# Performance work log

Measured on AMD Instinct MI355X. Metric: run time of the kernel, lower is better.

The kernel has to match this reference:

```python
import jax, jax.numpy as jnp
import numpy as np

N_NODES = 100000
N_EDGES = 1600000
N_GRAPHS = 1024
HID = 128
FINAL = 128
SPATIAL = 3
NUM_LAYERS = 3
VOCAB = 100


def _linear_params(key, d_in, d_out):
    k1, k2 = jax.random.split(key)
    s = 1.0 / np.sqrt(d_in)
    W = jax.random.uniform(k1, (d_out, d_in), jnp.float32, -s, s)
    b = jax.random.uniform(k2, (d_out,), jnp.float32, -s, s)
    return W, b


def setup_inputs() -> dict:
    key = jax.random.key(0)
    ks = jax.random.split(key, 16)
    z = jax.random.randint(ks[0], (N_NODES,), 0, VOCAB)
    pos = jax.random.normal(ks[1], (N_NODES, SPATIAL), jnp.float32)
    edge_index = jax.random.randint(ks[2], (2, N_EDGES), 0, N_NODES)
    batch = jnp.sort(jax.random.randint(ks[3], (N_NODES,), 0, N_GRAPHS))
    emb_table = jax.random.normal(ks[4], (VOCAB, HID), jnp.float32)
    W_pos, b_pos = _linear_params(ks[5], SPATIAL, HID)
    W_comb, b_comb = _linear_params(ks[6], 2 * HID, HID)
    # GIN: each conv's MLP is Linear(d,d) -> ReLU -> Linear(d,d); all dims 128 here.
    gW1, gb1, gW2, gb2 = [], [], [], []
    for i in range(NUM_LAYERS):
        k = jax.random.fold_in(ks[7], i)
        ka, kb = jax.random.split(k)
        W1, b1 = _linear_params(ka, HID, HID)
        W2, b2 = _linear_params(kb, HID, FINAL if i == NUM_LAYERS - 1 else HID)
        gW1.append(W1); gb1.append(b1); gW2.append(W2); gb2.append(b2)
    gin_W1 = jnp.stack(gW1); gin_b1 = jnp.stack(gb1)
    gin_W2 = jnp.stack(gW2); gin_b2 = jnp.stack(gb2)
    W_p1, b_p1 = _linear_params(ks[8], FINAL, FINAL)
    W_p2, b_p2 = _linear_params(ks[9], FINAL, 1)
    return {
        "z": z, "pos": pos, "edge_index": edge_index, "batch": batch,
        "emb_table": emb_table, "W_pos": W_pos, "b_pos": b_pos,
        "W_comb": W_comb, "b_comb": b_comb,
        "gin_W1": gin_W1, "gin_b1": gin_b1, "gin_W2": gin_W2, "gin_b2": gin_b2,
        "W_p1": W_p1, "b_p1": b_p1, "W_p2": W_p2, "b_p2": b_p2,
    }


def reference(z, pos, edge_index, batch, emb_table, W_pos, b_pos, W_comb, b_comb,
              gin_W1, gin_b1, gin_W2, gin_b2, W_p1, b_p1, W_p2, b_p2):
    src, dst = edge_index[0], edge_index[1]
    # initial node embedding: embed(z) || linear(pos) -> linear -> relu
    atom = emb_table[z]                                   # [N, H]
    pe = pos @ W_pos.T + b_pos                            # [N, H]
    x = jax.nn.relu(jnp.concatenate([atom, pe], axis=-1) @ W_comb.T + b_comb)
    # GIN layers: x' = MLP((1+eps)*x + sum_{j->i} x_j), eps=0; act between convs only
    for i in range(NUM_LAYERS):
        aggr = jax.ops.segment_sum(x[src], dst, num_segments=N_NODES)  # [N, H]
        h = aggr + x
        h = jax.nn.relu(h @ gin_W1[i].T + gin_b1[i])
        x = h @ gin_W2[i].T + gin_b2[i]
        if i < NUM_LAYERS - 1:
            x = jax.nn.relu(x)
    # sum pooling per graph, then predict MLP
    g = jax.ops.segment_sum(x, batch, num_segments=N_GRAPHS)  # [G, F]
    h = jax.nn.relu(g @ W_p1.T + b_p1)
    return h @ W_p2.T + b_p2                              # [G, 1]
```

## Files before the change

kernel.cpp:

```cpp
#include <hip/hip_runtime.h>
#include <hip/hip_bf16.h>

#define HID 128
#define CAP 64
#define NBK 2048
#define NWC 192

typedef __attribute__((ext_vector_type(8))) short bfrag;
typedef __attribute__((ext_vector_type(4))) float f32x4;

static inline size_t align256(size_t x) { return (x + 255) & ~(size_t)255; }

__device__ __forceinline__ unsigned short f2bf(float f) {
  unsigned int x = __float_as_uint(f);
  unsigned int r = x + 0x7fffu + ((x >> 16) & 1u);
  return (unsigned short)(r >> 16);
}
__device__ __forceinline__ float bflo(unsigned int u) { return __uint_as_float(u << 16); }
__device__ __forceinline__ float bfhi(unsigned int u) { return __uint_as_float(u & 0xffff0000u); }

__device__ __forceinline__ bfrag load8bf(const float* __restrict__ p) {
  const float4 a = *(const float4*)p;
  const float4 b = *(const float4*)(p + 4);
  bfrag r;
  r[0] = (short)f2bf(a.x); r[1] = (short)f2bf(a.y);
  r[2] = (short)f2bf(a.z); r[3] = (short)f2bf(a.w);
  r[4] = (short)f2bf(b.x); r[5] = (short)f2bf(b.y);
  r[6] = (short)f2bf(b.z); r[7] = (short)f2bf(b.w);
  return r;
}


__global__ __launch_bounds__(256, 2) void k_mega(
    const int* __restrict__ src, const int* __restrict__ dst,
    int* __restrict__ cnt, int* __restrict__ bsrc, int E, int N,
    const float* __restrict__ gW1, const float* __restrict__ gW2,
    unsigned short* __restrict__ W1b, unsigned short* __restrict__ W2b,
    const int* __restrict__ batch, int* __restrict__ goff, int G, int initBase,
    const int* __restrict__ z, const float* __restrict__ pos,
    const float* __restrict__ emb, const float* __restrict__ W_pos,
    const float* __restrict__ b_pos, const float* __restrict__ W_comb,
    const float* __restrict__ b_comb,
    unsigned int* __restrict__ UbZ, unsigned int* __restrict__ VbZ,
    unsigned short* __restrict__ Y, int n) {
  __shared__ unsigned int sE[32 * 128];
  __shared__ unsigned int sB[32 * 64];
  const int bid = blockIdx.x;
  const int tid = threadIdx.x;

  if (bid < NBK) {
    const int slice = bid & 7;
    const int sidx = bid >> 3;
    const int s_lo = (int)(((long long)slice * N) >> 3);
    const int s_hi = (int)(((long long)(slice + 1) * N) >> 3);
    for (int e = sidx * 256 + tid; e < E; e += (NBK / 8) * 256) {
      int d = dst[e];
      if (d >= s_lo && d < s_hi) {
        int slot = atomicAdd(&cnt[d], 1);
        if (slot < CAP) bsrc[(size_t)d * CAP + slot] = src[e];
      }
    }
    return;
  }
  if (bid < NBK + NWC) {
    int i = (bid - NBK) * 256 + tid;
    if (i < 3 * 128 * 128) {
      W1b[i] = f2bf(gW1[i]);
      W2b[i] = f2bf(gW2[i]);
    }
    return;
  }
  if (bid < initBase) {
    int g = (bid - NBK - NWC) * 256 + tid;
    if (g <= G) {
      int lo = 0, hi = N;
      while (lo < hi) {
        int mid = (lo + hi) >> 1;
        if (batch[mid] < g) lo = mid + 1; else hi = mid;
      }
      goff[g] = lo;
    }
    if (bid == initBase - 1) {
      if (tid >= 64 && tid < 128) UbZ[tid - 64] = 0;
      else if (tid >= 128 && tid < 192) VbZ[tid - 128] = 0;
    }
    return;
  }

  const int w = tid >> 6, l = tid & 63, lr = l & 15, lk = l >> 4;

  bfrag wcf[2][8];
#pragma unroll
  for (int s = 0; s < 2; ++s)
#pragma unroll
    for (int ks = 0; ks < 8; ++ks)
      wcf[s][ks] = load8bf(&W_comb[(size_t)(32 * w + 16 * s + lr) * 256 + ks * 32 + lk * 8]);
  bfrag w1f[2][4];
#pragma unroll
  for (int s = 0; s < 2; ++s)
#pragma unroll
    for (int ks = 0; ks < 4; ++ks)
      w1f[s][ks] = load8bf(&gW1[(size_t)(32 * w + 16 * s + lr) * HID + ks * 32 + lk * 8]);
  const float bias0 = b_comb[32 * w + lr];
  const float bias1 = b_comb[32 * w + 16 + lr];

  const int m0 = (bid - initBase) * 32;
  {
    const int r = tid >> 3, i = tid & 7;
    int node = m0 + r;
    if (node >= n) node = n - 1;
    const int zz = z[node];
    const float p0 = pos[node * 3 + 0], p1 = pos[node * 3 + 1], p2 = pos[node * 3 + 2];
    const int swz = (r & 7) << 2;
#pragma unroll
    for (int k = 0; k < 16; ++k) {
      const int j = i + k * 8;
      float v0, v1;
      if (j < 64) {
        const float2 ev = *(const float2*)&emb[(size_t)zz * 128 + 2 * j];
        v0 = ev.x; v1 = ev.y;
      } else {
        const int f0 = 2 * j - 128;
        v0 = b_pos[f0] + W_pos[f0 * 3] * p0 + W_pos[f0 * 3 + 1] * p1 + W_pos[f0 * 3 + 2] * p2;
        v1 = b_pos[f0 + 1] + W_pos[f0 * 3 + 3] * p0 + W_pos[f0 * 3 + 4] * p1 +
             W_pos[f0 * 3 + 5] * p2;
      }
      sE[r * 128 + (j ^ swz)] = (unsigned int)f2bf(v0) | ((unsigned int)f2bf(v1) << 16);
    }
  }
  __syncthreads();

  f32x4 acc00 = {0.f, 0.f, 0.f, 0.f}, acc01 = acc00, acc10 = acc00, acc11 = acc00;
#pragma unroll
  for (int mt = 0; mt < 2; ++mt) {
    const int row = 16 * mt + lr;
    const int swz = (row & 7) << 2;
#pragma unroll
    for (int ks = 0; ks < 8; ++ks) {
      const bfrag a = *(const bfrag*)&sE[row * 128 + ((ks * 16 + lk * 4) ^ swz)];
      if (mt == 0) {
        acc00 = __builtin_amdgcn_mfma_f32_16x16x32_bf16(a, wcf[0][ks], acc00, 0, 0, 0);
        acc01 = __builtin_amdgcn_mfma_f32_16x16x32_bf16(a, wcf[1][ks], acc01, 0, 0, 0);
      } else {
        acc10 = __builtin_amdgcn_mfma_f32_16x16x32_bf16(a, wcf[0][ks], acc10, 0, 0, 0);
        acc11 = __builtin_amdgcn_mfma_f32_16x16x32_bf16(a, wcf[1][ks], acc11, 0, 0, 0);
      }
    }
  }
  {
    unsigned short* sB16 = (unsigned short*)sB;
#pragma unroll
    for (int mt = 0; mt < 2; ++mt) {
#pragma unroll
      for (int s = 0; s < 2; ++s) {
        const f32x4 a = mt == 0 ? (s == 0 ? acc00 : acc01) : (s == 0 ? acc10 : acc11);
        const float bb = s == 0 ? bias0 : bias1;
        const int col = 32 * w + 16 * s + lr;
#pragma unroll
        for (int r = 0; r < 4; ++r) {
          const int rowL = 16 * mt + 4 * lk + r;
          const int cu = (col >> 1) ^ ((rowL & 7) << 2);
          sB16[rowL * 128 + cu * 2 + (col & 1)] = f2bf(fmaxf(a[r] + bb, 0.f));
        }
      }
    }
  }
  __syncthreads();

  f32x4 u00 = {0.f, 0.f, 0.f, 0.f}, u01 = u00, u10 = u00, u11 = u00;
#pragma unroll
  for (int mt = 0; mt < 2; ++mt) {
    const int row = 16 * mt + lr;
    const int swz = (row & 7) << 2;
#pragma unroll
    for (int ks = 0; ks < 4; ++ks) {
      const bfrag a = *(const bfrag*)&sB[row * 64 + ((ks * 16 + lk * 4) ^ swz)];
      if (mt == 0) {
        u00 = __builtin_amdgcn_mfma_f32_16x16x32_bf16(a, w1f[0][ks], u00, 0, 0, 0);
        u01 = __builtin_amdgcn_mfma_f32_16x16x32_bf16(a, w1f[1][ks], u01, 0, 0, 0);
      } else {
        u10 = __builtin_amdgcn_mfma_f32_16x16x32_bf16(a, w1f[0][ks], u10, 0, 0, 0);
        u11 = __builtin_amdgcn_mfma_f32_16x16x32_bf16(a, w1f[1][ks], u11, 0, 0, 0);
      }
    }
  }
#pragma unroll
  for (int mt = 0; mt < 2; ++mt) {
#pragma unroll
    for (int s = 0; s < 2; ++s) {
      const f32x4 a = mt == 0 ? (s == 0 ? u00 : u01) : (s == 0 ? u10 : u11);
      const int col = 32 * w + 16 * s + lr;
#pragma unroll
      for (int r = 0; r < 4; ++r) {
        const int row = m0 + 16 * mt + 4 * lk + r;
        if (row < n) Y[(size_t)row * HID + col] = f2bf(a[r]);
      }
    }
  }
}


template <int LAST>
__global__ __launch_bounds__(256, 3) void k_layer(const unsigned int* __restrict__ U,
                                                  const int* __restrict__ cnt,
                                                  const int* __restrict__ bsrc,
                                                  const float* __restrict__ b1,
                                                  const unsigned short* __restrict__ W2b,
                                                  const float* __restrict__ b2,
                                                  const unsigned short* __restrict__ W1n,
                                                  unsigned short* __restrict__ Y, int n) {
  __shared__ unsigned int sA[32 * 64];
  __shared__ unsigned int sB[32 * 64];
  const int t = threadIdx.x;
  const int w = t >> 6, l = t & 63, lr = l & 15, lk = l >> 4;
  const int lgrp = lk, lpos = lr;

  bfrag w2f[2][4];
#pragma unroll
  for (int s = 0; s < 2; ++s)
#pragma unroll
    for (int ks = 0; ks < 4; ++ks)
      w2f[s][ks] = *(const bfrag*)(W2b + (size_t)(32 * w + 16 * s + lr) * HID + ks * 32 + lk * 8);
  bfrag w1f[2][4];
  if (!LAST) {
#pragma unroll
    for (int s = 0; s < 2; ++s)
#pragma unroll
      for (int ks = 0; ks < 4; ++ks)
        w1f[s][ks] = *(const bfrag*)(W1n + (size_t)(32 * w + 16 * s + lr) * HID + ks * 32 + lk * 8);
  }
  const float b2a = b2[32 * w + lr];
  const float b2b = b2[32 * w + 16 + lr];
  const float4 bb0 = *(const float4*)&b1[8 * lpos];
  const float4 bb1 = *(const float4*)&b1[8 * lpos + 4];
  const float ms = (lgrp == 0) ? 1.f : 0.f;

  const int m0 = blockIdx.x * 32;

  int degs[8];
  int eidxs[8];
#pragma unroll
  for (int ri = 0; ri < 8; ++ri) {
    int node = m0 + 8 * w + ri;
    if (node >= n) node = n - 1;
    int d = cnt[node];
    d = d > CAP ? CAP : d;
    degs[ri] = d;
    const int e = bsrc[(size_t)node * CAP + l];
    eidxs[ri] = (l < d) ? e : n;
  }
#pragma unroll
  for (int ri = 0; ri < 8; ++ri) {
    const int row = 8 * w + ri;
    int node = m0 + row;
    if (node >= n) node = n - 1;
    const int deg8 = (degs[ri] + 7) & ~7;
    const int eidx = eidxs[ri];
    const uint4 sv = *(const uint4*)(U + (size_t)node * 64 + 4 * lpos);
    float a0 = ms * bflo(sv.x), a1 = ms * bfhi(sv.x);
    float a2 = ms * bflo(sv.y), a3 = ms * bfhi(sv.y);
    float a4 = ms * bflo(sv.z), a5 = ms * bfhi(sv.z);
    float a6 = ms * bflo(sv.w), a7 = ms * bfhi(sv.w);
    for (int k = 0; k < deg8; k += 8) {
      const int e0 = __shfl(eidx, k + lgrp);
      const int e1 = __shfl(eidx, k + 4 + lgrp);
      const uint4 u0 = *(const uint4*)(U + (size_t)e0 * 64 + 4 * lpos);
      const uint4 u1 = *(const uint4*)(U + (size_t)e1 * 64 + 4 * lpos);
      a0 += bflo(u0.x); a1 += bfhi(u0.x); a2 += bflo(u0.y); a3 += bfhi(u0.y);
      a4 += bflo(u0.z); a5 += bfhi(u0.z); a6 += bflo(u0.w); a7 += bfhi(u0.w);
      a0 += bflo(u1.x); a1 += bfhi(u1.x); a2 += bflo(u1.y); a3 += bfhi(u1.y);
      a4 += bflo(u1.z); a5 += bfhi(u1.z); a6 += bflo(u1.w); a7 += bfhi(u1.w);
    }
    a0 += __shfl_xor(a0, 16); a0 += __shfl_xor(a0, 32);
    a1 += __shfl_xor(a1, 16); a1 += __shfl_xor(a1, 32);
    a2 += __shfl_xor(a2, 16); a2 += __shfl_xor(a2, 32);
    a3 += __shfl_xor(a3, 16); a3 += __shfl_xor(a3, 32);
    a4 += __shfl_xor(a4, 16); a4 += __shfl_xor(a4, 32);
    a5 += __shfl_xor(a5, 16); a5 += __shfl_xor(a5, 32);
    a6 += __shfl_xor(a6, 16); a6 += __shfl_xor(a6, 32);
    a7 += __shfl_xor(a7, 16); a7 += __shfl_xor(a7, 32);
    if (lgrp == 0) {
      const int swz = (row & 7) << 2;
      uint4 o;
      o.x = (unsigned int)f2bf(fmaxf(a0 + bb0.x, 0.f)) |
            ((unsigned int)f2bf(fmaxf(a1 + bb0.y, 0.f)) << 16);
      o.y = (unsigned int)f2bf(fmaxf(a2 + bb0.z, 0.f)) |
            ((unsigned int)f2bf(fmaxf(a3 + bb0.w, 0.f)) << 16);
      o.z = (unsigned int)f2bf(fmaxf(a4 + bb1.x, 0.f)) |
            ((unsigned int)f2bf(fmaxf(a5 + bb1.y, 0.f)) << 16);
      o.w = (unsigned int)f2bf(fmaxf(a6 + bb1.z, 0.f)) |
            ((unsigned int)f2bf(fmaxf(a7 + bb1.w, 0.f)) << 16);
      *(uint4*)&sA[row * 64 + ((4 * lpos) ^ swz)] = o;
    }
  }
  __syncthreads();

  f32x4 acc00 = {0.f, 0.f, 0.f, 0.f}, acc01 = acc00, acc10 = acc00, acc11 = acc00;
#pragma unroll
  for (int mt = 0; mt < 2; ++mt) {
    const int row = 16 * mt + lr;
    const int swz = (row & 7) << 2;
#pragma unroll
    for (int ks = 0; ks < 4; ++ks) {
      const bfrag a = *(const bfrag*)&sA[row * 64 + ((ks * 16 + lk * 4) ^ swz)];
      if (mt == 0) {
        acc00 = __builtin_amdgcn_mfma_f32_16x16x32_bf16(a, w2f[0][ks], acc00, 0, 0, 0);
        acc01 = __builtin_amdgcn_mfma_f32_16x16x32_bf16(a, w2f[1][ks], acc01, 0, 0, 0);
      } else {
        acc10 = __builtin_amdgcn_mfma_f32_16x16x32_bf16(a, w2f[0][ks], acc10, 0, 0, 0);
        acc11 = __builtin_amdgcn_mfma_f32_16x16x32_bf16(a, w2f[1][ks], acc11, 0, 0, 0);
      }
    }
  }
  if (LAST) {
#pragma unroll
    for (int mt = 0; mt < 2; ++mt) {
#pragma unroll
      for (int s = 0; s < 2; ++s) {
        const f32x4 a = mt == 0 ? (s == 0 ? acc00 : acc01) : (s == 0 ? acc10 : acc11);
        const float bb = s == 0 ? b2a : b2b;
        const int col = 32 * w + 16 * s + lr;
#pragma unroll
        for (int r = 0; r < 4; ++r) {
          const int row = m0 + 16 * mt + 4 * lk + r;
          if (row < n) Y[(size_t)row * HID + col] = f2bf(a[r] + bb);
        }
      }
    }
  } else {
    unsigned short* sB16 = (unsigned short*)sB;
#pragma unroll
    for (int mt = 0; mt < 2; ++mt) {
#pragma unroll
      for (int s = 0; s < 2; ++s) {
        const f32x4 a = mt == 0 ? (s == 0 ? acc00 : acc01) : (s == 0 ? acc10 : acc11);
        const float bb = s == 0 ? b2a : b2b;
        const int col = 32 * w + 16 * s + lr;
#pragma unroll
        for (int r = 0; r < 4; ++r) {
          const int rowL = 16 * mt + 4 * lk + r;
          const int cu = (col >> 1) ^ ((rowL & 7) << 2);
          sB16[rowL * 128 + cu * 2 + (col & 1)] = f2bf(fmaxf(a[r] + bb, 0.f));
        }
      }
    }
    __syncthreads();
    f32x4 u00 = {0.f, 0.f, 0.f, 0.f}, u01 = u00, u10 = u00, u11 = u00;
#pragma unroll
    for (int mt = 0; mt < 2; ++mt) {
      const int row = 16 * mt + lr;
      const int swz = (row & 7) << 2;
#pragma unroll
      for (int ks = 0; ks < 4; ++ks) {
        const bfrag a = *(const bfrag*)&sB[row * 64 + ((ks * 16 + lk * 4) ^ swz)];
        if (mt == 0) {
          u00 = __builtin_amdgcn_mfma_f32_16x16x32_bf16(a, w1f[0][ks], u00, 0, 0, 0);
          u01 = __builtin_amdgcn_mfma_f32_16x16x32_bf16(a, w1f[1][ks], u01, 0, 0, 0);
        } else {
          u10 = __builtin_amdgcn_mfma_f32_16x16x32_bf16(a, w1f[0][ks], u10, 0, 0, 0);
          u11 = __builtin_amdgcn_mfma_f32_16x16x32_bf16(a, w1f[1][ks], u11, 0, 0, 0);
        }
      }
    }
#pragma unroll
    for (int mt = 0; mt < 2; ++mt) {
#pragma unroll
      for (int s = 0; s < 2; ++s) {
        const f32x4 a = mt == 0 ? (s == 0 ? u00 : u01) : (s == 0 ? u10 : u11);
        const int col = 32 * w + 16 * s + lr;
#pragma unroll
        for (int r = 0; r < 4; ++r) {
          const int row = m0 + 16 * mt + 4 * lk + r;
          if (row < n) Y[(size_t)row * HID + col] = f2bf(a[r]);
        }
      }
    }
  }
}


__global__ __launch_bounds__(128) void k_pool(const unsigned short* __restrict__ X,
                                              const int* __restrict__ goff,
                                              const float* __restrict__ Wp1,
                                              const float* __restrict__ bp1,
                                              const float* __restrict__ Wp2,
                                              const float* __restrict__ bp2,
                                              float* __restrict__ out, int G) {
  __shared__ float sg[HID];
  __shared__ float sred[HID];
  int g = blockIdx.x;
  int f = threadIdx.x;
  int n0 = goff[g], n1 = goff[g + 1];
  float c0 = 0.f, c1 = 0.f, c2 = 0.f, c3 = 0.f;
  int nn = n0;
  for (; nn + 3 < n1; nn += 4) {
    c0 += __uint_as_float((unsigned int)X[(size_t)nn * HID + f] << 16);
    c1 += __uint_as_float((unsigned int)X[(size_t)(nn + 1) * HID + f] << 16);
    c2 += __uint_as_float((unsigned int)X[(size_t)(nn + 2) * HID + f] << 16);
    c3 += __uint_as_float((unsigned int)X[(size_t)(nn + 3) * HID + f] << 16);
  }
  for (; nn < n1; ++nn) c0 += __uint_as_float((unsigned int)X[(size_t)nn * HID + f] << 16);
  sg[f] = (c0 + c1) + (c2 + c3);
  __syncthreads();
  float a0 = 0.f, a1 = 0.f, a2 = 0.f, a3 = 0.f;
#pragma unroll
  for (int k4 = 0; k4 < 32; ++k4) {
    float4 wv = *(const float4*)&Wp1[f * HID + k4 * 4];
    float4 xv = *(const float4*)&sg[k4 * 4];
    a0 += wv.x * xv.x; a1 += wv.y * xv.y; a2 += wv.z * xv.z; a3 += wv.w * xv.w;
  }
  float h = fmaxf(bp1[f] + ((a0 + a1) + (a2 + a3)), 0.f);
  sred[f] = Wp2[f] * h;
  __syncthreads();
  for (int s = 64; s > 0; s >>= 1) {
    if (f < s) sred[f] += sred[f + s];
    __syncthreads();
  }
  if (f == 0) out[g] = sred[0] + bp2[0];
}


extern "C" void kernel_launch(void* const* d_in, const int* in_sizes, int n_in,
                              void* d_out, int out_size, void* d_ws, size_t ws_size,
                              hipStream_t stream) {
  const int*   z      = (const int*)d_in[0];
  const float* pos    = (const float*)d_in[1];
  const int*   ei     = (const int*)d_in[2];
  const int*   batch  = (const int*)d_in[3];
  const float* emb    = (const float*)d_in[4];
  const float* W_pos  = (const float*)d_in[5];
  const float* b_pos  = (const float*)d_in[6];
  const float* W_comb = (const float*)d_in[7];
  const float* b_comb = (const float*)d_in[8];
  const float* gW1    = (const float*)d_in[9];
  const float* gb1    = (const float*)d_in[10];
  const float* gW2    = (const float*)d_in[11];
  const float* gb2    = (const float*)d_in[12];
  const float* Wp1    = (const float*)d_in[13];
  const float* bp1    = (const float*)d_in[14];
  const float* Wp2    = (const float*)d_in[15];
  const float* bp2    = (const float*)d_in[16];
  float* out = (float*)d_out;

  const int N = in_sizes[0];
  const int E = in_sizes[2] / 2;
  const int G = out_size;
  const int* srcp = ei;
  const int* dstp = ei + E;
  const int ntiles = (N + 31) / 32;
  const int nGoff = (G + 1 + 255) / 256;
  const int initBase = NBK + NWC + nGoff;

  char* w = (char*)d_ws;
  unsigned short* Ub  = (unsigned short*)w; w += align256((size_t)(N + 1) * 128 * 2);
  unsigned short* Vb  = (unsigned short*)w; w += align256((size_t)(N + 1) * 128 * 2);
  unsigned short* W1b = (unsigned short*)w; w += align256((size_t)3 * 128 * 128 * 2);
  unsigned short* W2b = (unsigned short*)w; w += align256((size_t)3 * 128 * 128 * 2);
  int* cnt  = (int*)w; w += align256((size_t)N * 4);
  int* bsrc = (int*)w; w += align256((size_t)N * CAP * 4);
  int* goff = (int*)w; w += align256((size_t)(G + 1) * 4);

  hipMemsetAsync(cnt, 0, (size_t)N * 4, stream);

  k_mega<<<initBase + ntiles, 256, 0, stream>>>(
      srcp, dstp, cnt, bsrc, E, N, gW1, gW2, W1b, W2b, batch, goff, G, initBase,
      z, pos, emb, W_pos, b_pos, W_comb, b_comb,
      (unsigned int*)(Ub + (size_t)N * 128), (unsigned int*)(Vb + (size_t)N * 128), Ub, N);

  k_layer<0><<<ntiles, 256, 0, stream>>>((const unsigned int*)Ub, cnt, bsrc, gb1,
                                         W2b, gb2, W1b + (size_t)1 * 128 * 128, Vb, N);
  k_layer<0><<<ntiles, 256, 0, stream>>>((const unsigned int*)Vb, cnt, bsrc, gb1 + 128,
                                         W2b + (size_t)1 * 128 * 128, gb2 + 128,
                                         W1b + (size_t)2 * 128 * 128, Ub, N);
  k_layer<1><<<ntiles, 256, 0, stream>>>((const unsigned int*)Ub, cnt, bsrc, gb1 + 256,
                                         W2b + (size_t)2 * 128 * 128, gb2 + 256,
                                         (const unsigned short*)nullptr, Vb, N);

  k_pool<<<G, HID, 0, stream>>>(Vb, goff, Wp1, bp1, Wp2, bp2, out, G);
}
```

Baseline: 483.9 us.

## Split mega prep kernel into separate prep and init-matmul kernels; raise layer occupancy

```diff
diff --git a/kernel.cpp b/kernel.cpp
--- a/kernel.cpp
+++ b/kernel.cpp
@@ -31,23 +31,20 @@
 }
 
 
-__global__ __launch_bounds__(256, 2) void k_mega(
-    const int* __restrict__ src, const int* __restrict__ dst,
-    int* __restrict__ cnt, int* __restrict__ bsrc, int E, int N,
-    const float* __restrict__ gW1, const float* __restrict__ gW2,
-    unsigned short* __restrict__ W1b, unsigned short* __restrict__ W2b,
-    const int* __restrict__ batch, int* __restrict__ goff, int G, int initBase,
-    const int* __restrict__ z, const float* __restrict__ pos,
-    const float* __restrict__ emb, const float* __restrict__ W_pos,
-    const float* __restrict__ b_pos, const float* __restrict__ W_comb,
-    const float* __restrict__ b_comb,
-    unsigned int* __restrict__ UbZ, unsigned int* __restrict__ VbZ,
-    unsigned short* __restrict__ Y, int n) {
-  __shared__ unsigned int sE[32 * 128];
-  __shared__ unsigned int sB[32 * 64];
+__global__ __launch_bounds__(256) void k_prep(const int* __restrict__ src,
+                                              const int* __restrict__ dst,
+                                              int* __restrict__ cnt,
+                                              int* __restrict__ bsrc, int E, int N,
+                                              const float* __restrict__ gW1,
+                                              const float* __restrict__ gW2,
+                                              unsigned short* __restrict__ W1b,
+                                              unsigned short* __restrict__ W2b,
+                                              const int* __restrict__ batch,
+                                              int* __restrict__ goff, int G,
+                                              unsigned int* __restrict__ UbZ,
+                                              unsigned int* __restrict__ VbZ) {
   const int bid = blockIdx.x;
   const int tid = threadIdx.x;
-
   if (bid < NBK) {
     const int slice = bid & 7;
     const int sidx = bid >> 3;
@@ -60,17 +57,13 @@
         if (slot < CAP) bsrc[(size_t)d * CAP + slot] = src[e];
       }
     }
-    return;
-  }
-  if (bid < NBK + NWC) {
+  } else if (bid < NBK + NWC) {
     int i = (bid - NBK) * 256 + tid;
     if (i < 3 * 128 * 128) {
       W1b[i] = f2bf(gW1[i]);
       W2b[i] = f2bf(gW2[i]);
     }
-    return;
-  }
-  if (bid < initBase) {
+  } else {
     int g = (bid - NBK - NWC) * 256 + tid;
     if (g <= G) {
       int lo = 0, hi = N;
@@ -80,14 +73,27 @@
       }
       goff[g] = lo;
     }
-    if (bid == initBase - 1) {
+    if (bid == NBK + NWC) {
       if (tid >= 64 && tid < 128) UbZ[tid - 64] = 0;
       else if (tid >= 128 && tid < 192) VbZ[tid - 128] = 0;
     }
-    return;
-  }
-
-  const int w = tid >> 6, l = tid & 63, lr = l & 15, lk = l >> 4;
+  }
+}
+
+
+__global__ __launch_bounds__(256, 2) void k_init_mm(const int* __restrict__ z,
+                                                    const float* __restrict__ pos,
+                                                    const float* __restrict__ emb,
+                                                    const float* __restrict__ W_pos,
+                                                    const float* __restrict__ b_pos,
+                                                    const float* __restrict__ W_comb,
+                                                    const float* __restrict__ b_comb,
+                                                    const float* __restrict__ gW1,
+                                                    unsigned short* __restrict__ Y, int n) {
+  __shared__ unsigned int sE[32 * 128];
+  __shared__ unsigned int sB[32 * 64];
+  const int t = threadIdx.x;
+  const int w = t >> 6, l = t & 63, lr = l & 15, lk = l >> 4;
 
   bfrag wcf[2][8];
 #pragma unroll
@@ -104,9 +110,9 @@
   const float bias0 = b_comb[32 * w + lr];
   const float bias1 = b_comb[32 * w + 16 + lr];
 
-  const int m0 = (bid - initBase) * 32;
+  const int m0 = blockIdx.x * 32;
   {
-    const int r = tid >> 3, i = tid & 7;
+    const int r = t >> 3, i = t & 7;
     int node = m0 + r;
     if (node >= n) node = n - 1;
     const int zz = z[node];
@@ -201,7 +207,7 @@
 
 
 template <int LAST>
-__global__ __launch_bounds__(256, 3) void k_layer(const unsigned int* __restrict__ U,
+__global__ __launch_bounds__(256, 4) void k_layer(const unsigned int* __restrict__ U,
                                                   const int* __restrict__ cnt,
                                                   const int* __restrict__ bsrc,
                                                   const float* __restrict__ b1,
@@ -449,7 +455,6 @@
   const int* dstp = ei + E;
   const int ntiles = (N + 31) / 32;
   const int nGoff = (G + 1 + 255) / 256;
-  const int initBase = NBK + NWC + nGoff;
 
   char* w = (char*)d_ws;
   unsigned short* Ub  = (unsigned short*)w; w += align256((size_t)(N + 1) * 128 * 2);
@@ -462,10 +467,12 @@
 
   hipMemsetAsync(cnt, 0, (size_t)N * 4, stream);
 
-  k_mega<<<initBase + ntiles, 256, 0, stream>>>(
-      srcp, dstp, cnt, bsrc, E, N, gW1, gW2, W1b, W2b, batch, goff, G, initBase,
-      z, pos, emb, W_pos, b_pos, W_comb, b_comb,
-      (unsigned int*)(Ub + (size_t)N * 128), (unsigned int*)(Vb + (size_t)N * 128), Ub, N);
+  k_prep<<<NBK + NWC + nGoff, 256, 0, stream>>>(
+      srcp, dstp, cnt, bsrc, E, N, gW1, gW2, W1b, W2b, batch, goff, G,
+      (unsigned int*)(Ub + (size_t)N * 128), (unsigned int*)(Vb + (size_t)N * 128));
+
+  k_init_mm<<<ntiles, 256, 0, stream>>>(z, pos, emb, W_pos, b_pos, W_comb, b_comb,
+                                        gW1, Ub, N);
 
   k_layer<0><<<ntiles, 256, 0, stream>>>((const unsigned int*)Ub, cnt, bsrc, gb1,
                                          W2b, gb2, W1b + (size_t)1 * 128 * 128, Vb, N);
```

After: 439.0 us. 9.3% less time.
